# Kernel tuning notes

Hardware: AMD Instinct MI355X
Metric: run time of the kernel (lower is better)

Reference implementation:

```python
import jax, jax.numpy as jnp
import numpy as np

N, NFEAT, NHID, NHEADS, OUT_DIM = 4096, 512, 64, 8, 512
ALPHA = 0.2      # LeakyReLU negative slope
NEG = -9e15      # masked-out logit value (as in pyGAT)


def setup_inputs() -> dict:
    key = jax.random.key(0)
    ks = jax.random.split(key, 10)
    s = 0.1
    x = jax.random.normal(ks[0], (N, NFEAT), jnp.float32)
    adj = jax.random.randint(ks[1], (N, N), 0, 2, jnp.int32)  # dense 0/1 adjacency
    W1 = jax.random.normal(ks[2], (NHEADS, NFEAT, NHID), jnp.float32) * s
    a1 = jax.random.normal(ks[3], (NHEADS, 2 * NHID), jnp.float32) * s
    Wo = jax.random.normal(ks[4], (NHEADS * NHID, OUT_DIM), jnp.float32) * s
    ao = jax.random.normal(ks[5], (2 * OUT_DIM,), jnp.float32) * s
    lin1_w = jax.random.normal(ks[6], (OUT_DIM, 1024), jnp.float32) * s
    lin1_b = jnp.zeros((1024,), jnp.float32)
    lin2_w = jax.random.normal(ks[7], (1024, 512), jnp.float32) * s
    lin2_b = jnp.zeros((512,), jnp.float32)
    return dict(x=x, adj=adj, W1=W1, a1=a1, Wo=Wo, ao=ao,
                lin1_w=lin1_w, lin1_b=lin1_b, lin2_w=lin2_w, lin2_b=lin2_b)


def _gat_heads(x, adj_mask, W, a):
    # Dense pyGAT GraphAttentionLayer, vectorized over heads.
    # W: [H, F, O], a: [H, 2O], x: [N, F], adj_mask: [N, N] bool
    O = W.shape[-1]
    Wh = jnp.einsum('nf,hfo->hno', x, W)                      # [H, N, O]
    src = jnp.einsum('hno,ho->hn', Wh, a[:, :O])              # a_1^T Wh_i
    dst = jnp.einsum('hno,ho->hn', Wh, a[:, O:])              # a_2^T Wh_j
    e = jax.nn.leaky_relu(src[:, :, None] + dst[:, None, :], ALPHA)  # [H, N, N]
    e = jnp.where(adj_mask[None, :, :], e, NEG)
    attn = jax.nn.softmax(e, axis=-1)
    return jnp.einsum('hnm,hmo->hno', attn, Wh)               # [H, N, O]


def reference(x, adj, W1, a1, Wo, ao, lin1_w, lin1_b, lin2_w, lin2_b):
    mask = adj > 0
    # layer-1 heads (concat=True -> elu per head), then concat along features
    h = jax.nn.elu(_gat_heads(x, mask, W1, a1))               # [H, N, NHID]
    x1 = jnp.transpose(h, (1, 0, 2)).reshape(x.shape[0], -1)  # [N, H*NHID]
    # output attention head (concat=False -> raw h'), elu applied in GAT.forward
    h2 = _gat_heads(x1, mask, Wo[None], ao[None])[0]          # [N, OUT_DIM]
    out = jax.nn.elu(h2)
    out = jax.nn.relu(out @ lin1_w + lin1_b)                  # Linear(out_dim,1024)+ReLU
    return out @ lin2_w + lin2_b                              # Linear(1024,512)
```

## Files before the change

kernel.cpp:

```cpp
#include <hip/hip_runtime.h>

#define NN 4096
#define NFEAT 512
#define NHID 64
#define NHEADS 8
#define OUTD 512
#define LRALPHA 0.2f
#define NSPLIT 2
#define JS (NN / NSPLIT)
#define JTILES (JS / 64)

typedef __attribute__((ext_vector_type(4))) float f32x4;
typedef __attribute__((ext_vector_type(8))) short short8;
typedef __attribute__((ext_vector_type(4))) int   int4v;
typedef __attribute__((ext_vector_type(2))) unsigned uint2v;

#define OFF_BITS (size_t)0x0
#define OFF_WHA  (size_t)0x200000
#define OFF_SRC  (size_t)0xA00000
#define OFF_DST  (size_t)0xA20000
#define OFF_MDM  (size_t)0xA40000
#define OFF_MDD  (size_t)0xA80000
#define OFF_XHH  (size_t)0xAC0000
#define OFF_XHL  (size_t)0xEC0000
#define OFF_WHH  (size_t)0x12C0000
#define OFF_WHL  (size_t)0x16C0000
#define OFF_PART (size_t)0x1AC0000
#define OFF_L1OH OFF_PART
#define OFF_L1OL (OFF_PART + (size_t)0x800000)
#define OFF_W1TH (size_t)0x2AC0000
#define OFF_W1TL (size_t)0x2B40000
#define OFF_WOTH (size_t)0x2BC0000
#define OFF_WOTL (size_t)0x2C40000
#define OFF_L1WH (size_t)0x2CC0000
#define OFF_L1WL (size_t)0x2DC0000
#define OFF_L2WH (size_t)0x2EC0000
#define OFF_L2WL (size_t)0x2FC0000

__device__ inline unsigned short f2bf(float x) {
    unsigned u = __float_as_uint(x);
    return (unsigned short)((u + 0x7FFFu + ((u >> 16) & 1u)) >> 16);
}

#define PACK_PAIR(ve, vo, hw_, lw_) {                                   \
    unsigned ue = __float_as_uint(ve), uo = __float_as_uint(vo);        \
    unsigned ho = uo & 0xFFFF0000u;                                     \
    hw_ = (int)(ho | (ue >> 16));                                       \
    float le_ = (ve) - __uint_as_float(ue & 0xFFFF0000u);               \
    float lo_ = (vo) - __uint_as_float(ho);                             \
    lw_ = (int)((__float_as_uint(lo_) & 0xFFFF0000u) |                  \
                (__float_as_uint(le_) >> 16)); }

__global__ __launch_bounds__(256) void pack_bits_kernel(
    const int* __restrict__ adj, unsigned int* __restrict__ bits)
{
    int wid  = (blockIdx.x * 256 + threadIdx.x) >> 6;
    int lane = threadIdx.x & 63;
    int row  = wid >> 6;
    int j0   = (wid & 63) << 6;
    int v    = adj[(long)row * NN + j0 + lane];
    unsigned long long m = __ballot(v > 0);
    if (lane == 0)  bits[row * 128 + (j0 >> 5)]     = (unsigned int)m;
    if (lane == 32) bits[row * 128 + (j0 >> 5) + 1] = (unsigned int)(m >> 32);
}

__global__ __launch_bounds__(256) void splitA_kernel(
    const float* __restrict__ in, unsigned short* __restrict__ oh,
    unsigned short* __restrict__ ol)
{
    long i = ((long)blockIdx.x * 256 + threadIdx.x) * 8;
    float4 a = *(const float4*)&in[i], b = *(const float4*)&in[i + 4];
    float v[8] = {a.x, a.y, a.z, a.w, b.x, b.y, b.z, b.w};
    int4v hw, lw;
    #pragma unroll
    for (int pp = 0; pp < 4; ++pp) PACK_PAIR(v[2*pp], v[2*pp+1], hw[pp], lw[pp]);
    *(short8*)&oh[i] = __builtin_bit_cast(short8, hw);
    *(short8*)&ol[i] = __builtin_bit_cast(short8, lw);
}

__global__ __launch_bounds__(256) void splitBT_kernel(
    const float* __restrict__ B, unsigned short* __restrict__ oh,
    unsigned short* __restrict__ ol, int K, int N, long srcZ, long dstZ)
{
    __shared__ float tile[64][65];
    const int t = threadIdx.x;
    const int n0 = blockIdx.x * 64, k0 = blockIdx.y * 64;
    B  += srcZ * blockIdx.z;
    oh += dstZ * blockIdx.z;
    ol += dstZ * blockIdx.z;
    #pragma unroll
    for (int it = 0; it < 4; ++it) {
        int k = it * 16 + (t >> 4);
        *(float4*)&tile[k][(t & 15) * 4] =
            *(const float4*)&B[(long)(k0 + k) * N + n0 + (t & 15) * 4];
    }
    __syncthreads();
    const int n = t >> 2, kc = (t & 3) * 16;
    #pragma unroll
    for (int g = 0; g < 2; ++g) {
        int4v hw, lw;
        #pragma unroll
        for (int pp = 0; pp < 4; ++pp) {
            float ve = tile[kc + g * 8 + 2 * pp][n];
            float vo = tile[kc + g * 8 + 2 * pp + 1][n];
            PACK_PAIR(ve, vo, hw[pp], lw[pp]);
        }
        long ob = (long)(n0 + n) * K + k0 + kc + g * 8;
        *(short8*)&oh[ob] = __builtin_bit_cast(short8, hw);
        *(short8*)&ol[ob] = __builtin_bit_cast(short8, lw);
    }
}

template<int WF32, int WSPL, int DO_BIAS, int DO_RELU>
__global__ __launch_bounds__(256, 3) void mgemm_kernel(
    const unsigned short* __restrict__ Ah, const unsigned short* __restrict__ Al,
    const unsigned short* __restrict__ Bh, const unsigned short* __restrict__ Bl,
    float* __restrict__ C, unsigned short* __restrict__ Ch,
    unsigned short* __restrict__ Cl, const float* __restrict__ bias,
    int N, int K, long bZ, long cZ)
{
    __shared__ unsigned short AH[2][4096], AL[2][4096];
    __shared__ unsigned short BH[2][2048], BL[2][2048];

    const int t = threadIdx.x;
    const int m0 = blockIdx.x * 128, n0 = blockIdx.y * 64;
    Bh += bZ * blockIdx.z; Bl += bZ * blockIdx.z;
    if (WF32) C += cZ * blockIdx.z;

    const int ar0 = t >> 2, ar1 = 64 + (t >> 2), akb = t & 3;
    const unsigned short* pAh = Ah + (long)(m0 + ar0) * K + akb * 8;
    const unsigned short* pAl = Al + (long)(m0 + ar0) * K + akb * 8;
    const unsigned short* pBh = Bh + (long)(n0 + ar0) * K + akb * 8;
    const unsigned short* pBl = Bl + (long)(n0 + ar0) * K + akb * 8;
    const long aRow1 = (long)64 * K;
    const int adst0 = ar0 * 32 + ((akb ^ ((ar0 >> 1) & 3)) << 3);
    const int adst1 = ar1 * 32 + ((akb ^ ((ar1 >> 1) & 3)) << 3);
    const int bdst  = adst0;

    short8 sh0, sh1, sl0, sl1, sbh, sbl;
    const int S = K / 32;

#define MG_LOAD(s) { long o = (long)(s) * 32;                     \
        sh0 = *(const short8*)(pAh + o);                          \
        sh1 = *(const short8*)(pAh + aRow1 + o);                  \
        sl0 = *(const short8*)(pAl + o);                          \
        sl1 = *(const short8*)(pAl + aRow1 + o);                  \
        sbh = *(const short8*)(pBh + o);                          \
        sbl = *(const short8*)(pBl + o); }
#define MG_COMMIT(b) {                                            \
        *(short8*)&AH[b][adst0] = sh0; *(short8*)&AH[b][adst1] = sh1; \
        *(short8*)&AL[b][adst0] = sl0; *(short8*)&AL[b][adst1] = sl1; \
        *(short8*)&BH[b][bdst]  = sbh; *(short8*)&BL[b][bdst]  = sbl; }

    MG_LOAD(0);
    MG_COMMIT(0);
    if (S > 1) MG_LOAD(1);
    __syncthreads();

    const int w = t >> 6, l = t & 63;
    const int kb = l >> 4;
    const int r0 = w * 32 + (l & 15), r1 = r0 + 16;
    const int ao0 = r0 * 32 + ((kb ^ ((r0 >> 1) & 3)) << 3);
    const int ao1 = r1 * 32 + ((kb ^ ((r1 >> 1) & 3)) << 3);

    f32x4 acc0[4] = {}, acc1[4] = {};

    for (int s = 0; s < S; ++s) {
        const int cur = s & 1;
        if (s + 1 < S) MG_COMMIT(cur ^ 1);
        if (s + 2 < S) MG_LOAD(s + 2);

        short8 a0h = *(const short8*)&AH[cur][ao0];
        short8 a0l = *(const short8*)&AL[cur][ao0];
        short8 a1h = *(const short8*)&AH[cur][ao1];
        short8 a1l = *(const short8*)&AL[cur][ao1];
        #pragma unroll
        for (int ct = 0; ct < 4; ++ct) {
            const int n = ct * 16 + (l & 15);
            const int bo = n * 32 + ((kb ^ ((n >> 1) & 3)) << 3);
            short8 bh = *(const short8*)&BH[cur][bo];
            short8 bl = *(const short8*)&BL[cur][bo];
            acc0[ct] = __builtin_amdgcn_mfma_f32_16x16x32_bf16(a0h, bh, acc0[ct], 0, 0, 0);
            acc0[ct] = __builtin_amdgcn_mfma_f32_16x16x32_bf16(a0h, bl, acc0[ct], 0, 0, 0);
            acc0[ct] = __builtin_amdgcn_mfma_f32_16x16x32_bf16(a0l, bh, acc0[ct], 0, 0, 0);
            acc1[ct] = __builtin_amdgcn_mfma_f32_16x16x32_bf16(a1h, bh, acc1[ct], 0, 0, 0);
            acc1[ct] = __builtin_amdgcn_mfma_f32_16x16x32_bf16(a1h, bl, acc1[ct], 0, 0, 0);
            acc1[ct] = __builtin_amdgcn_mfma_f32_16x16x32_bf16(a1l, bh, acc1[ct], 0, 0, 0);
        }
        __syncthreads();
    }
#undef MG_LOAD
#undef MG_COMMIT

    #pragma unroll
    for (int rs = 0; rs < 2; ++rs) {
        #pragma unroll
        for (int ct = 0; ct < 4; ++ct) {
            const int col = n0 + ct * 16 + (l & 15);
            float b = DO_BIAS ? bias[col] : 0.f;
            f32x4 av = rs ? acc1[ct] : acc0[ct];
            #pragma unroll
            for (int g = 0; g < 4; ++g) {
                int row = m0 + w * 32 + rs * 16 + (l >> 4) * 4 + g;
                float v = av[g] + b;
                if (DO_RELU) v = v > 0.f ? v : 0.f;
                if (WF32) C[(long)row * N + col] = v;
                if (WSPL) {
                    unsigned u = __float_as_uint(v);
                    Ch[(long)row * N + col] = (unsigned short)(u >> 16);
                    float lo = v - __uint_as_float(u & 0xFFFF0000u);
                    Cl[(long)row * N + col] = (unsigned short)(__float_as_uint(lo) >> 16);
                }
            }
        }
    }
}

__global__ __launch_bounds__(256) void srcdst_kernel(
    const float* __restrict__ Wh, const float* __restrict__ a,
    float* __restrict__ src, float* __restrict__ dst, int HN, int Nn, int O)
{
    int wid  = (blockIdx.x * 256 + threadIdx.x) >> 6;
    int lane = threadIdx.x & 63;
    if (wid >= HN) return;
    int h = wid / Nn;
    const float* row = Wh + (long)wid * O;
    const float* ah  = a + (long)h * 2 * O;
    float s = 0.f, d = 0.f;
    for (int o = lane; o < O; o += 64) {
        float v = row[o];
        s += v * ah[o];
        d += v * ah[O + o];
    }
    #pragma unroll
    for (int off = 32; off > 0; off >>= 1) {
        s += __shfl_xor(s, off);
        d += __shfl_xor(d, off);
    }
    if (lane == 0) { src[wid] = s; dst[wid] = d; }
}

__global__ __launch_bounds__(256) void whsplit_kernel(
    const float* __restrict__ Wh, long yStride, int ldJ,
    unsigned short* __restrict__ outH, unsigned short* __restrict__ outL)
{
    __shared__ float tile[64][68];
    const int t = threadIdx.x;
    const int j0 = blockIdx.x * 64;
    const int y = blockIdx.y;
    #pragma unroll
    for (int p = 0; p < 4; ++p) {
        int j = p * 16 + (t >> 4);
        int c = (t & 15) * 4;
        *(float4*)&tile[j][c] =
            *(const float4*)&Wh[(long)(j0 + j) * ldJ + (long)y * yStride + c];
    }
    __syncthreads();
    const int c = t >> 2, jb = (t & 3) * 16;
    short8 H0, H1, L0, L1;
    #pragma unroll
    for (int e = 0; e < 8; ++e) {
        float v = tile[jb + e][c];
        unsigned short h = f2bf(v);
        H0[e] = (short)h;
        L0[e] = (short)f2bf(v - __uint_as_float((unsigned)h << 16));
    }
    #pragma unroll
    for (int e = 0; e < 8; ++e) {
        float v = tile[jb + 8 + e][c];
        unsigned short h = f2bf(v);
        H1[e] = (short)h;
        L1[e] = (short)f2bf(v - __uint_as_float((unsigned)h << 16));
    }
    long ob = (long)y * 262144 + (long)c * 4096 + j0 + jb;
    *(short8*)&outH[ob]     = H0;
    *(short8*)&outH[ob + 8] = H1;
    *(short8*)&outL[ob]     = L0;
    *(short8*)&outL[ob + 8] = L1;
}

__global__ __launch_bounds__(512, 4) void attn_kernel(
    const unsigned short* __restrict__ whH, const unsigned short* __restrict__ whL,
    const float* __restrict__ src, const float* __restrict__ dst, int snOff_y,
    const unsigned int* __restrict__ bits,
    float* __restrict__ partA, float* __restrict__ md_m, float* __restrict__ md_d)
{
    __shared__ unsigned short BH[2][4096];
    __shared__ unsigned short BL[2][4096];
    __shared__ float dstS[JS];
    __shared__ float srcS[128], mS[128];

    const int t  = threadIdx.x;
    const int i0 = blockIdx.x * 128;
    const int y  = blockIdx.y;
    const int js = blockIdx.z;
    src += (long)snOff_y * y;
    dst += (long)snOff_y * y;

    const int sc = t >> 3, sb = t & 7;
    const long gbase = (long)y * 262144 + (long)sc * 4096 + js * JS + sb * 8;
    const int sdst = sc * 64 + ((sb ^ (sc & 7)) << 3);

    short8 stH = *(const short8*)(whH + gbase);
    short8 stL = *(const short8*)(whL + gbase);

    *(float4*)&dstS[t * 4] = *(const float4*)&dst[js * JS + t * 4];
    if (t < 128) srcS[t] = src[i0 + t];
    __syncthreads();

    {
        const int r = t >> 2, q = t & 3;
        float md = -3.0e38f;
        const unsigned int* brow = bits + (long)(i0 + r) * 128 + js * (JS / 32) + q * 16;
        for (int wi = 0; wi < 16; ++wi) {
            unsigned int b = brow[wi];
            if (!b) continue;
            int base = q * 512 + wi * 32;
            while (b) {
                int bi = __ffs(b) - 1; b &= b - 1;
                float v = dstS[base + bi];
                md = v > md ? v : md;
            }
        }
        md = fmaxf(md, __shfl_xor(md, 1));
        md = fmaxf(md, __shfl_xor(md, 2));
        if (q == 0) {
            float m;
            if (md < -2.9e38f) m = -2.0e38f;
            else { float e = srcS[r] + md; m = e > 0.f ? e : LRALPHA * e; }
            mS[r] = m;
        }
    }
    *(short8*)&BH[0][sdst] = stH;
    *(short8*)&BL[0][sdst] = stL;
    stH = *(const short8*)(whH + gbase + 64);
    stL = *(const short8*)(whL + gbase + 64);
    __syncthreads();

    const int w = t >> 6, l = t & 63;
    const int rA = 16 * w + (l & 15);
    const int q8 = (l >> 4) * 8;
    const float src_r = srcS[rA];
    const float m_r   = mS[rA];
    const bool  empty = (m_r <= -1.9e38f);
    const unsigned int* browp = bits + (long)(i0 + rA) * 128 + js * (JS / 32);
    const short8 ONES = {(short)0x3F80, (short)0x3F80, (short)0x3F80, (short)0x3F80,
                         (short)0x3F80, (short)0x3F80, (short)0x3F80, (short)0x3F80};

    f32x4 acc[4] = {};
    f32x4 acc_d = {};

    for (int jt = 0; jt < JTILES; ++jt) {
        const int cur = jt & 1;
        if (jt + 1 < JTILES) {
            *(short8*)&BH[cur ^ 1][sdst] = stH;
            *(short8*)&BL[cur ^ 1][sdst] = stL;
        }
        if (jt + 2 < JTILES) {
            stH = *(const short8*)(whH + gbase + (jt + 2) * 64);
            stL = *(const short8*)(whL + gbase + (jt + 2) * 64);
        }
        unsigned int bw0 = browp[jt * 2], bw1 = browp[jt * 2 + 1];
        short8 aH0, aL0, aH1, aL1;
        #pragma unroll
        for (int kt = 0; kt < 2; ++kt) {
            unsigned int bw = kt ? bw1 : bw0;
            float4 d0 = *(const float4*)&dstS[jt * 64 + kt * 32 + q8];
            float4 d1 = *(const float4*)&dstS[jt * 64 + kt * 32 + q8 + 4];
            float dv[8] = {d0.x, d0.y, d0.z, d0.w, d1.x, d1.y, d1.z, d1.w};
            float pv[8];
            #pragma unroll
            for (int e = 0; e < 8; ++e) {
                float v = src_r + dv[e];
                v = fmaxf(v, LRALPHA * v);
                float pe = __expf(v - m_r);
                bool valid = (bw >> (q8 + e)) & 1u;
                pv[e] = empty ? 1.f : (valid ? pe : 0.f);
            }
            int4v hw, lw;
            #pragma unroll
            for (int pp = 0; pp < 4; ++pp) PACK_PAIR(pv[2*pp], pv[2*pp+1], hw[pp], lw[pp]);
            short8 aH = __builtin_bit_cast(short8, hw);
            short8 aL = __builtin_bit_cast(short8, lw);
            acc_d = __builtin_amdgcn_mfma_f32_16x16x32_bf16(aH, ONES, acc_d, 0, 0, 0);
            acc_d = __builtin_amdgcn_mfma_f32_16x16x32_bf16(aL, ONES, acc_d, 0, 0, 0);
            if (kt == 0) { aH0 = aH; aL0 = aL; } else { aH1 = aH; aL1 = aL; }
        }
        #pragma unroll
        for (int kt = 0; kt < 2; ++kt) {
            short8 aH = kt ? aH1 : aH0;
            short8 aL = kt ? aL1 : aL0;
            #pragma unroll
            for (int ct = 0; ct < 4; ++ct) {
                const int c = ct * 16 + (l & 15);
                const int off = c * 64 + ((((kt * 4) + (l >> 4)) ^ (c & 7)) << 3);
                short8 bh = *(const short8*)&BH[cur][off];
                short8 bl = *(const short8*)&BL[cur][off];
                acc[ct] = __builtin_amdgcn_mfma_f32_16x16x32_bf16(aH, bh, acc[ct], 0, 0, 0);
                acc[ct] = __builtin_amdgcn_mfma_f32_16x16x32_bf16(aH, bl, acc[ct], 0, 0, 0);
                acc[ct] = __builtin_amdgcn_mfma_f32_16x16x32_bf16(aL, bh, acc[ct], 0, 0, 0);
            }
        }
        __syncthreads();
    }

    const int colb = y * 64 + (l & 15);
    #pragma unroll
    for (int ct = 0; ct < 4; ++ct) {
        #pragma unroll
        for (int g = 0; g < 4; ++g) {
            int row = 16 * w + (l >> 4) * 4 + g;
            partA[((long)js * NN + i0 + row) * OUTD + colb + ct * 16] = acc[ct][g];
        }
    }
    if ((l & 15) == 0) {
        long mdoff = ((long)js * NHEADS + y) * NN + i0 + 16 * w + (l >> 4) * 4;
        #pragma unroll
        for (int g = 0; g < 4; ++g) md_d[mdoff + g] = acc_d[g];
    }
    if (l < 16) {
        md_m[((long)js * NHEADS + y) * NN + i0 + 16 * w + l] = m_r;
    }
}

__global__ __launch_bounds__(256) void combine_kernel(
    const float* __restrict__ partA, const float* __restrict__ md_m,
    const float* __restrict__ md_d, unsigned short* __restrict__ outH,
    unsigned short* __restrict__ outL)
{
    int idx4 = (blockIdx.x * 256 + threadIdx.x) * 4;
    int row  = idx4 >> 9;
    int col  = idx4 & 511;
    int slot = col >> 6;
    float m[NSPLIT], w[NSPLIT];
    float M = -3.4e38f;
    #pragma unroll
    for (int s = 0; s < NSPLIT; ++s) {
        m[s] = md_m[((long)s * NHEADS + slot) * NN + row];
        M = fmaxf(M, m[s]);
    }
    float den = 0.f;
    #pragma unroll
    for (int s = 0; s < NSPLIT; ++s) {
        w[s] = __expf(m[s] - M);
        den += w[s] * md_d[((long)s * NHEADS + slot) * NN + row];
    }
    float4 num = {0.f, 0.f, 0.f, 0.f};
    #pragma unroll
    for (int s = 0; s < NSPLIT; ++s) {
        float4 a = *(const float4*)&partA[((long)s * NN + row) * OUTD + col];
        num.x += w[s] * a.x; num.y += w[s] * a.y;
        num.z += w[s] * a.z; num.w += w[s] * a.w;
    }
    float inv = 1.f / den;
    float o[4]; const float* pn = &num.x;
    #pragma unroll
    for (int j = 0; j < 4; ++j) {
        float v = pn[j] * inv;
        o[j] = v > 0.f ? v : (__expf(v) - 1.f);
    }
    int h0, h1, l0, l1;
    PACK_PAIR(o[0], o[1], h0, l0);
    PACK_PAIR(o[2], o[3], h1, l1);
    uint2v hv = {(unsigned)h0, (unsigned)h1};
    uint2v lv = {(unsigned)l0, (unsigned)l1};
    *(uint2v*)&outH[(long)row * OUTD + col] = hv;
    *(uint2v*)&outL[(long)row * OUTD + col] = lv;
}

extern "C" void kernel_launch(void* const* d_in, const int* in_sizes, int n_in,
                              void* d_out, int out_size, void* d_ws, size_t ws_size,
                              hipStream_t stream) {
    const float* x   = (const float*)d_in[0];
    const int*   adj = (const int*)d_in[1];
    const float* W1  = (const float*)d_in[2];
    const float* a1  = (const float*)d_in[3];
    const float* Wo  = (const float*)d_in[4];
    const float* ao  = (const float*)d_in[5];
    const float* l1w = (const float*)d_in[6];
    const float* l1b = (const float*)d_in[7];
    const float* l2w = (const float*)d_in[8];
    const float* l2b = (const float*)d_in[9];
    float* out = (float*)d_out;

    char* ws = (char*)d_ws;
    unsigned int* bits = (unsigned int*)(ws + OFF_BITS);
    float* WhA  = (float*)(ws + OFF_WHA);
    float* srcB = (float*)(ws + OFF_SRC);
    float* dstB = (float*)(ws + OFF_DST);
    float* mdm  = (float*)(ws + OFF_MDM);
    float* mdd  = (float*)(ws + OFF_MDD);
    unsigned short* xhH = (unsigned short*)(ws + OFF_XHH);
    unsigned short* xhL = (unsigned short*)(ws + OFF_XHL);
    unsigned short* whH = (unsigned short*)(ws + OFF_WHH);
    unsigned short* whL = (unsigned short*)(ws + OFF_WHL);
    float* part = (float*)(ws + OFF_PART);
    unsigned short* l1oH = (unsigned short*)(ws + OFF_L1OH);
    unsigned short* l1oL = (unsigned short*)(ws + OFF_L1OL);
    unsigned short* w1tH = (unsigned short*)(ws + OFF_W1TH);
    unsigned short* w1tL = (unsigned short*)(ws + OFF_W1TL);
    unsigned short* wotH = (unsigned short*)(ws + OFF_WOTH);
    unsigned short* wotL = (unsigned short*)(ws + OFF_WOTL);
    unsigned short* l1wH = (unsigned short*)(ws + OFF_L1WH);
    unsigned short* l1wL = (unsigned short*)(ws + OFF_L1WL);
    unsigned short* l2wH = (unsigned short*)(ws + OFF_L2WH);
    unsigned short* l2wL = (unsigned short*)(ws + OFF_L2WL);

    pack_bits_kernel<<<65536, 256, 0, stream>>>(adj, bits);
    splitA_kernel<<<1024, 256, 0, stream>>>(x, xhH, xhL);
    splitBT_kernel<<<dim3(1, 8, 8), 256, 0, stream>>>(W1, w1tH, w1tL, NFEAT, NHID,
        (long)NFEAT * NHID, (long)NHID * NFEAT);
    splitBT_kernel<<<dim3(8, 8, 1), 256, 0, stream>>>(Wo, wotH, wotL, 512, OUTD, 0, 0);
    splitBT_kernel<<<dim3(16, 8, 1), 256, 0, stream>>>(l1w, l1wH, l1wL, OUTD, 1024, 0, 0);
    splitBT_kernel<<<dim3(8, 16, 1), 256, 0, stream>>>(l2w, l2wH, l2wL, 1024, OUTD, 0, 0);

    mgemm_kernel<1,0,0,0><<<dim3(32, 1, 8), 256, 0, stream>>>(
        xhH, xhL, w1tH, w1tL, WhA, nullptr, nullptr, nullptr,
        NHID, NFEAT, (long)NHID * NFEAT, (long)NN * NHID);
    srcdst_kernel<<<8192, 256, 0, stream>>>(WhA, a1, srcB, dstB, NHEADS*NN, NN, NHID);
    whsplit_kernel<<<dim3(64, 8), 256, 0, stream>>>(WhA, (long)NN*NHID, NHID, whH, whL);
    attn_kernel<<<dim3(32, 8, NSPLIT), 512, 0, stream>>>(
        whH, whL, srcB, dstB, NN, bits, part, mdm, mdd);
    combine_kernel<<<2048, 256, 0, stream>>>(part, mdm, mdd, xhH, xhL);
    mgemm_kernel<1,0,0,0><<<dim3(32, 8, 1), 256, 0, stream>>>(
        xhH, xhL, wotH, wotL, WhA, nullptr, nullptr, nullptr, OUTD, 512, 0, 0);
    srcdst_kernel<<<1024, 256, 0, stream>>>(WhA, ao, srcB, dstB, NN, NN, OUTD);
    whsplit_kernel<<<dim3(64, 8), 256, 0, stream>>>(WhA, 64L, OUTD, whH, whL);
    attn_kernel<<<dim3(32, 8, NSPLIT), 512, 0, stream>>>(
        whH, whL, srcB, dstB, 0, bits, part, mdm, mdd);
    combine_kernel<<<2048, 256, 0, stream>>>(part, mdm, mdd, xhH, xhL);
    mgemm_kernel<0,1,1,1><<<dim3(32, 16, 1), 256, 0, stream>>>(
        xhH, xhL, l1wH, l1wL, nullptr, l1oH, l1oL, l1b, 1024, OUTD, 0, 0);
    mgemm_kernel<1,0,1,0><<<dim3(32, 8, 1), 256, 0, stream>>>(
        l1oH, l1oL, l2wH, l2wL, out, nullptr, nullptr, l2b, OUTD, 1024, 0, 0);
}
```

Before: 462.5 us.

## Fuse src/dst and bf16 split into GEMM epilogue, widen attention split, use exp2

The Wh GEMM epilogue now computes the attention src/dst dot products (pre-scaled by log2e) and writes the transposed bf16 hi/lo split directly, removing the separate srcdst and whsplit kernels and the fp32 Wh round trip. The output layer accumulates src/dst with atomics into a buffer zeroed by a new kernel. The attention j-range is split four ways when the workspace is large enough, which raises parallelism at the cost of more combine traffic. Float-to-bf16 packing switches to the hardware packed-convert instruction, and the exponentials use exp2 with masking folded into the exponent argument.

```diff
diff --git a/kernel.cpp b/kernel.cpp
--- a/kernel.cpp
+++ b/kernel.cpp
@@ -6,9 +6,7 @@
 #define NHEADS 8
 #define OUTD 512
 #define LRALPHA 0.2f
-#define NSPLIT 2
-#define JS (NN / NSPLIT)
-#define JTILES (JS / 64)
+#define LOG2E 1.4426950408889634f
 
 typedef __attribute__((ext_vector_type(4))) float f32x4;
 typedef __attribute__((ext_vector_type(8))) short short8;
@@ -16,40 +14,48 @@
 typedef __attribute__((ext_vector_type(2))) unsigned uint2v;
 
 #define OFF_BITS (size_t)0x0
-#define OFF_WHA  (size_t)0x200000
-#define OFF_SRC  (size_t)0xA00000
-#define OFF_DST  (size_t)0xA20000
-#define OFF_MDM  (size_t)0xA40000
-#define OFF_MDD  (size_t)0xA80000
-#define OFF_XHH  (size_t)0xAC0000
-#define OFF_XHL  (size_t)0xEC0000
-#define OFF_WHH  (size_t)0x12C0000
-#define OFF_WHL  (size_t)0x16C0000
-#define OFF_PART (size_t)0x1AC0000
+#define OFF_XHH  (size_t)0x200000
+#define OFF_XHL  (size_t)0x600000
+#define OFF_WHH  (size_t)0xA00000
+#define OFF_WHL  (size_t)0xE00000
+#define OFF_W1TH (size_t)0x1200000
+#define OFF_W1TL (size_t)0x1280000
+#define OFF_WOTH (size_t)0x1300000
+#define OFF_WOTL (size_t)0x1380000
+#define OFF_L1WH (size_t)0x1400000
+#define OFF_L1WL (size_t)0x1500000
+#define OFF_L2WH (size_t)0x1600000
+#define OFF_L2WL (size_t)0x1700000
+#define OFF_SRC  (size_t)0x1800000
+#define OFF_DST  (size_t)0x1820000
+#define OFF_SRC2 (size_t)0x1840000
+#define OFF_DST2 (size_t)0x1844000
+#define OFF_MDM  (size_t)0x1850000
+#define OFF_MDD  (size_t)0x18D0000
+#define OFF_PART (size_t)0x1950000
 #define OFF_L1OH OFF_PART
 #define OFF_L1OL (OFF_PART + (size_t)0x800000)
-#define OFF_W1TH (size_t)0x2AC0000
-#define OFF_W1TL (size_t)0x2B40000
-#define OFF_WOTH (size_t)0x2BC0000
-#define OFF_WOTL (size_t)0x2C40000
-#define OFF_L1WH (size_t)0x2CC0000
-#define OFF_L1WL (size_t)0x2DC0000
-#define OFF_L2WH (size_t)0x2EC0000
-#define OFF_L2WL (size_t)0x2FC0000
-
-__device__ inline unsigned short f2bf(float x) {
-    unsigned u = __float_as_uint(x);
-    return (unsigned short)((u + 0x7FFFu + ((u >> 16) & 1u)) >> 16);
-}
-
-#define PACK_PAIR(ve, vo, hw_, lw_) {                                   \
-    unsigned ue = __float_as_uint(ve), uo = __float_as_uint(vo);        \
-    unsigned ho = uo & 0xFFFF0000u;                                     \
-    hw_ = (int)(ho | (ue >> 16));                                       \
-    float le_ = (ve) - __uint_as_float(ue & 0xFFFF0000u);               \
-    float lo_ = (vo) - __uint_as_float(ho);                             \
-    lw_ = (int)((__float_as_uint(lo_) & 0xFFFF0000u) |                  \
-                (__float_as_uint(le_) >> 16)); }
+#define WS_NEED4 (OFF_PART + (size_t)0x2000000)
+#define WS_NEED2 (OFF_PART + (size_t)0x1000000)
+
+__device__ inline unsigned cvt_pk_bf16(float lo, float hi) {
+    unsigned r;
+    asm("v_cvt_pk_bf16_f32 %0, %1, %2" : "=v"(r) : "v"(lo), "v"(hi));
+    return r;
+}
+__device__ inline void pack_pair(float ve, float vo, unsigned& hw, unsigned& lw) {
+    hw = cvt_pk_bf16(ve, vo);
+    float he = __uint_as_float(hw << 16);
+    float ho = __uint_as_float(hw & 0xFFFF0000u);
+    lw = cvt_pk_bf16(ve - he, vo - ho);
+}
+__device__ inline float exp2_fast(float x) {
+#if __has_builtin(__builtin_amdgcn_exp2f)
+    return __builtin_amdgcn_exp2f(x);
+#else
+    float r; asm("v_exp_f32 %0, %1" : "=v"(r) : "v"(x)); return r;
+#endif
+}
 
 __global__ __launch_bounds__(256) void pack_bits_kernel(
     const int* __restrict__ adj, unsigned int* __restrict__ bits)
@@ -64,6 +70,13 @@
     if (lane == 32) bits[row * 128 + (j0 >> 5) + 1] = (unsigned int)(m >> 32);
 }
 
+__global__ __launch_bounds__(256) void zero_kernel(float* __restrict__ a,
+                                                   float* __restrict__ b)
+{
+    int i = blockIdx.x * 256 + threadIdx.x;
+    if (i < NN) { a[i] = 0.f; b[i] = 0.f; }
+}
+
 __global__ __launch_bounds__(256) void splitA_kernel(
     const float* __restrict__ in, unsigned short* __restrict__ oh,
     unsigned short* __restrict__ ol)
@@ -73,7 +86,10 @@
     float v[8] = {a.x, a.y, a.z, a.w, b.x, b.y, b.z, b.w};
     int4v hw, lw;
     #pragma unroll
-    for (int pp = 0; pp < 4; ++pp) PACK_PAIR(v[2*pp], v[2*pp+1], hw[pp], lw[pp]);
+    for (int pp = 0; pp < 4; ++pp) {
+        unsigned h, l; pack_pair(v[2*pp], v[2*pp+1], h, l);
+        hw[pp] = (int)h; lw[pp] = (int)l;
+    }
     *(short8*)&oh[i] = __builtin_bit_cast(short8, hw);
     *(short8*)&ol[i] = __builtin_bit_cast(short8, lw);
 }
@@ -101,9 +117,9 @@
         int4v hw, lw;
         #pragma unroll
         for (int pp = 0; pp < 4; ++pp) {
-            float ve = tile[kc + g * 8 + 2 * pp][n];
-            float vo = tile[kc + g * 8 + 2 * pp + 1][n];
-            PACK_PAIR(ve, vo, hw[pp], lw[pp]);
+            unsigned h, l;
+            pack_pair(tile[kc + g*8 + 2*pp][n], tile[kc + g*8 + 2*pp + 1][n], h, l);
+            hw[pp] = (int)h; lw[pp] = (int)l;
         }
         long ob = (long)(n0 + n) * K + k0 + kc + g * 8;
         *(short8*)&oh[ob] = __builtin_bit_cast(short8, hw);
@@ -111,21 +127,23 @@
     }
 }
 
-template<int WF32, int WSPL, int DO_BIAS, int DO_RELU>
+template<int EPI, int DO_BIAS, int DO_RELU>
 __global__ __launch_bounds__(256, 3) void mgemm_kernel(
     const unsigned short* __restrict__ Ah, const unsigned short* __restrict__ Al,
     const unsigned short* __restrict__ Bh, const unsigned short* __restrict__ Bl,
     float* __restrict__ C, unsigned short* __restrict__ Ch,
     unsigned short* __restrict__ Cl, const float* __restrict__ bias,
-    int N, int K, long bZ, long cZ)
+    const float* __restrict__ avec, float* __restrict__ srcO, float* __restrict__ dstO,
+    unsigned short* __restrict__ tH, unsigned short* __restrict__ tL,
+    int N, int K, long bZ, long cZ, int aoff)
 {
     __shared__ unsigned short AH[2][4096], AL[2][4096];
-    __shared__ unsigned short BH[2][2048], BL[2][2048];
+    __shared__ unsigned short BHs[2][2048], BLs[2][2048];
 
     const int t = threadIdx.x;
     const int m0 = blockIdx.x * 128, n0 = blockIdx.y * 64;
-    Bh += bZ * blockIdx.z; Bl += bZ * blockIdx.z;
-    if (WF32) C += cZ * blockIdx.z;
+    const int zi = blockIdx.z;
+    Bh += bZ * zi; Bl += bZ * zi;
 
     const int ar0 = t >> 2, ar1 = 64 + (t >> 2), akb = t & 3;
     const unsigned short* pAh = Ah + (long)(m0 + ar0) * K + akb * 8;
@@ -135,7 +153,6 @@
     const long aRow1 = (long)64 * K;
     const int adst0 = ar0 * 32 + ((akb ^ ((ar0 >> 1) & 3)) << 3);
     const int adst1 = ar1 * 32 + ((akb ^ ((ar1 >> 1) & 3)) << 3);
-    const int bdst  = adst0;
 
     short8 sh0, sh1, sl0, sl1, sbh, sbl;
     const int S = K / 32;
@@ -150,7 +167,7 @@
 #define MG_COMMIT(b) {                                            \
         *(short8*)&AH[b][adst0] = sh0; *(short8*)&AH[b][adst1] = sh1; \
         *(short8*)&AL[b][adst0] = sl0; *(short8*)&AL[b][adst1] = sl1; \
-        *(short8*)&BH[b][bdst]  = sbh; *(short8*)&BL[b][bdst]  = sbl; }
+        *(short8*)&BHs[b][adst0] = sbh; *(short8*)&BLs[b][adst0] = sbl; }
 
     MG_LOAD(0);
     MG_COMMIT(0);
@@ -178,8 +195,8 @@
         for (int ct = 0; ct < 4; ++ct) {
             const int n = ct * 16 + (l & 15);
             const int bo = n * 32 + ((kb ^ ((n >> 1) & 3)) << 3);
-            short8 bh = *(const short8*)&BH[cur][bo];
-            short8 bl = *(const short8*)&BL[cur][bo];
+            short8 bh = *(const short8*)&BHs[cur][bo];
+            short8 bl = *(const short8*)&BLs[cur][bo];
             acc0[ct] = __builtin_amdgcn_mfma_f32_16x16x32_bf16(a0h, bh, acc0[ct], 0, 0, 0);
             acc0[ct] = __builtin_amdgcn_mfma_f32_16x16x32_bf16(a0h, bl, acc0[ct], 0, 0, 0);
             acc0[ct] = __builtin_amdgcn_mfma_f32_16x16x32_bf16(a0l, bh, acc0[ct], 0, 0, 0);
@@ -192,102 +209,98 @@
 #undef MG_LOAD
 #undef MG_COMMIT
 
-    #pragma unroll
-    for (int rs = 0; rs < 2; ++rs) {
+    if constexpr (EPI <= 1) {
+        #pragma unroll
+        for (int rs = 0; rs < 2; ++rs) {
+            #pragma unroll
+            for (int ct = 0; ct < 4; ++ct) {
+                const int col = n0 + ct * 16 + (l & 15);
+                float b = DO_BIAS ? bias[col] : 0.f;
+                f32x4 av = rs ? acc1[ct] : acc0[ct];
+                #pragma unroll
+                for (int g = 0; g < 4; ++g) {
+                    int row = m0 + w * 32 + rs * 16 + (l >> 4) * 4 + g;
+                    float v = av[g] + b;
+                    if (DO_RELU) v = v > 0.f ? v : 0.f;
+                    if (EPI == 0) C[cZ * zi + (long)row * N + col] = v;
+                    else {
+                        unsigned u = __float_as_uint(v);
+                        Ch[(long)row * N + col] = (unsigned short)((u + 0x7FFFu + ((u >> 16) & 1u)) >> 16);
+                        unsigned hh = (u + 0x7FFFu + ((u >> 16) & 1u)) & 0xFFFF0000u;
+                        float hf = __uint_as_float(((u + 0x7FFFu + ((u >> 16) & 1u)) >> 16) << 16);
+                        float lo = v - hf;
+                        unsigned ul = __float_as_uint(lo);
+                        Cl[(long)row * N + col] = (unsigned short)((ul + 0x7FFFu + ((ul >> 16) & 1u)) >> 16);
+                        (void)hh;
+                    }
+                }
+            }
+        }
+    } else {
+        float avs[4], avd[4];
         #pragma unroll
         for (int ct = 0; ct < 4; ++ct) {
-            const int col = n0 + ct * 16 + (l & 15);
-            float b = DO_BIAS ? bias[col] : 0.f;
-            f32x4 av = rs ? acc1[ct] : acc0[ct];
+            int col = n0 + ct * 16 + (l & 15);
+            avs[ct] = avec[(EPI == 2 ? zi * 2 * 64 : 0) + col];
+            avd[ct] = avec[(EPI == 2 ? zi * 2 * 64 : 0) + aoff + col];
+        }
+        #pragma unroll
+        for (int rs = 0; rs < 2; ++rs) {
+            const int rbase = m0 + w * 32 + rs * 16 + (l >> 4) * 4;
+            #pragma unroll
+            for (int ct = 0; ct < 4; ++ct) {
+                const int col = n0 + ct * 16 + (l & 15);
+                f32x4 av = rs ? acc1[ct] : acc0[ct];
+                unsigned h0, l0, h1, l1;
+                pack_pair(av[0], av[1], h0, l0);
+                pack_pair(av[2], av[3], h1, l1);
+                long tb = (EPI == 2 ? (long)zi * 262144 + (long)col * 4096
+                                    : (long)(col >> 6) * 262144 + (long)(col & 63) * 4096)
+                          + rbase;
+                uint2v hv = {h0, h1}, lv = {l0, l1};
+                *(uint2v*)&tH[tb] = hv;
+                *(uint2v*)&tL[tb] = lv;
+            }
             #pragma unroll
             for (int g = 0; g < 4; ++g) {
-                int row = m0 + w * 32 + rs * 16 + (l >> 4) * 4 + g;
-                float v = av[g] + b;
-                if (DO_RELU) v = v > 0.f ? v : 0.f;
-                if (WF32) C[(long)row * N + col] = v;
-                if (WSPL) {
-                    unsigned u = __float_as_uint(v);
-                    Ch[(long)row * N + col] = (unsigned short)(u >> 16);
-                    float lo = v - __uint_as_float(u & 0xFFFF0000u);
-                    Cl[(long)row * N + col] = (unsigned short)(__float_as_uint(lo) >> 16);
+                float sd = 0.f, dd = 0.f;
+                #pragma unroll
+                for (int ct = 0; ct < 4; ++ct) {
+                    f32x4 av = rs ? acc1[ct] : acc0[ct];
+                    sd += av[g] * avs[ct];
+                    dd += av[g] * avd[ct];
                 }
-            }
-        }
-    }
-}
-
-__global__ __launch_bounds__(256) void srcdst_kernel(
-    const float* __restrict__ Wh, const float* __restrict__ a,
-    float* __restrict__ src, float* __restrict__ dst, int HN, int Nn, int O)
-{
-    int wid  = (blockIdx.x * 256 + threadIdx.x) >> 6;
-    int lane = threadIdx.x & 63;
-    if (wid >= HN) return;
-    int h = wid / Nn;
-    const float* row = Wh + (long)wid * O;
-    const float* ah  = a + (long)h * 2 * O;
-    float s = 0.f, d = 0.f;
-    for (int o = lane; o < O; o += 64) {
-        float v = row[o];
-        s += v * ah[o];
-        d += v * ah[O + o];
-    }
-    #pragma unroll
-    for (int off = 32; off > 0; off >>= 1) {
-        s += __shfl_xor(s, off);
-        d += __shfl_xor(d, off);
-    }
-    if (lane == 0) { src[wid] = s; dst[wid] = d; }
-}
-
-__global__ __launch_bounds__(256) void whsplit_kernel(
-    const float* __restrict__ Wh, long yStride, int ldJ,
-    unsigned short* __restrict__ outH, unsigned short* __restrict__ outL)
-{
-    __shared__ float tile[64][68];
-    const int t = threadIdx.x;
-    const int j0 = blockIdx.x * 64;
-    const int y = blockIdx.y;
-    #pragma unroll
-    for (int p = 0; p < 4; ++p) {
-        int j = p * 16 + (t >> 4);
-        int c = (t & 15) * 4;
-        *(float4*)&tile[j][c] =
-            *(const float4*)&Wh[(long)(j0 + j) * ldJ + (long)y * yStride + c];
-    }
-    __syncthreads();
-    const int c = t >> 2, jb = (t & 3) * 16;
-    short8 H0, H1, L0, L1;
-    #pragma unroll
-    for (int e = 0; e < 8; ++e) {
-        float v = tile[jb + e][c];
-        unsigned short h = f2bf(v);
-        H0[e] = (short)h;
-        L0[e] = (short)f2bf(v - __uint_as_float((unsigned)h << 16));
-    }
-    #pragma unroll
-    for (int e = 0; e < 8; ++e) {
-        float v = tile[jb + 8 + e][c];
-        unsigned short h = f2bf(v);
-        H1[e] = (short)h;
-        L1[e] = (short)f2bf(v - __uint_as_float((unsigned)h << 16));
-    }
-    long ob = (long)y * 262144 + (long)c * 4096 + j0 + jb;
-    *(short8*)&outH[ob]     = H0;
-    *(short8*)&outH[ob + 8] = H1;
-    *(short8*)&outL[ob]     = L0;
-    *(short8*)&outL[ob + 8] = L1;
-}
-
+                #pragma unroll
+                for (int off = 1; off < 16; off <<= 1) {
+                    sd += __shfl_xor(sd, off);
+                    dd += __shfl_xor(dd, off);
+                }
+                if ((l & 15) == 0) {
+                    int row = rbase + g;
+                    if (EPI == 2) {
+                        srcO[zi * NN + row] = sd * LOG2E;
+                        dstO[zi * NN + row] = dd * LOG2E;
+                    } else {
+                        atomicAdd(&srcO[row], sd * LOG2E);
+                        atomicAdd(&dstO[row], dd * LOG2E);
+                    }
+                }
+            }
+        }
+    }
+}
+
+template<int JS_>
 __global__ __launch_bounds__(512, 4) void attn_kernel(
     const unsigned short* __restrict__ whH, const unsigned short* __restrict__ whL,
     const float* __restrict__ src, const float* __restrict__ dst, int snOff_y,
     const unsigned int* __restrict__ bits,
     float* __restrict__ partA, float* __restrict__ md_m, float* __restrict__ md_d)
 {
+    constexpr int JT_ = JS_ / 64;
     __shared__ unsigned short BH[2][4096];
     __shared__ unsigned short BL[2][4096];
-    __shared__ float dstS[JS];
+    __shared__ float dstS[JS_];
     __shared__ float srcS[128], mS[128];
 
     const int t  = threadIdx.x;
@@ -298,24 +311,26 @@
     dst += (long)snOff_y * y;
 
     const int sc = t >> 3, sb = t & 7;
-    const long gbase = (long)y * 262144 + (long)sc * 4096 + js * JS + sb * 8;
+    const long gbase = (long)y * 262144 + (long)sc * 4096 + (long)js * JS_ + sb * 8;
     const int sdst = sc * 64 + ((sb ^ (sc & 7)) << 3);
 
     short8 stH = *(const short8*)(whH + gbase);
     short8 stL = *(const short8*)(whL + gbase);
 
-    *(float4*)&dstS[t * 4] = *(const float4*)&dst[js * JS + t * 4];
+    if (t * 4 < JS_)
+        *(float4*)&dstS[t * 4] = *(const float4*)&dst[(long)js * JS_ + t * 4];
     if (t < 128) srcS[t] = src[i0 + t];
     __syncthreads();
 
     {
+        constexpr int WPQ = JS_ / 128;
         const int r = t >> 2, q = t & 3;
         float md = -3.0e38f;
-        const unsigned int* brow = bits + (long)(i0 + r) * 128 + js * (JS / 32) + q * 16;
-        for (int wi = 0; wi < 16; ++wi) {
+        const unsigned int* brow = bits + (long)(i0 + r) * 128 + js * (JS_ / 32) + q * WPQ;
+        for (int wi = 0; wi < WPQ; ++wi) {
             unsigned int b = brow[wi];
             if (!b) continue;
-            int base = q * 512 + wi * 32;
+            int base = q * (JS_ / 4) + wi * 32;
             while (b) {
                 int bi = __ffs(b) - 1; b &= b - 1;
                 float v = dstS[base + bi];
@@ -327,7 +342,7 @@
         if (q == 0) {
             float m;
             if (md < -2.9e38f) m = -2.0e38f;
-            else { float e = srcS[r] + md; m = e > 0.f ? e : LRALPHA * e; }
+            else { float e = srcS[r] + md; m = fmaxf(e, LRALPHA * e); }
             mS[r] = m;
         }
     }
@@ -343,20 +358,20 @@
     const float src_r = srcS[rA];
     const float m_r   = mS[rA];
     const bool  empty = (m_r <= -1.9e38f);
-    const unsigned int* browp = bits + (long)(i0 + rA) * 128 + js * (JS / 32);
+    const unsigned int* browp = bits + (long)(i0 + rA) * 128 + js * (JS_ / 32);
     const short8 ONES = {(short)0x3F80, (short)0x3F80, (short)0x3F80, (short)0x3F80,
                          (short)0x3F80, (short)0x3F80, (short)0x3F80, (short)0x3F80};
 
     f32x4 acc[4] = {};
     f32x4 acc_d = {};
 
-    for (int jt = 0; jt < JTILES; ++jt) {
+    for (int jt = 0; jt < JT_; ++jt) {
         const int cur = jt & 1;
-        if (jt + 1 < JTILES) {
+        if (jt + 1 < JT_) {
             *(short8*)&BH[cur ^ 1][sdst] = stH;
             *(short8*)&BL[cur ^ 1][sdst] = stL;
         }
-        if (jt + 2 < JTILES) {
+        if (jt + 2 < JT_) {
             stH = *(const short8*)(whH + gbase + (jt + 2) * 64);
             stL = *(const short8*)(whL + gbase + (jt + 2) * 64);
         }
@@ -373,13 +388,18 @@
             for (int e = 0; e < 8; ++e) {
                 float v = src_r + dv[e];
                 v = fmaxf(v, LRALPHA * v);
-                float pe = __expf(v - m_r);
+                float s = v - m_r;
                 bool valid = (bw >> (q8 + e)) & 1u;
-                pv[e] = empty ? 1.f : (valid ? pe : 0.f);
+                s = valid ? s : -1.0e30f;
+                s = empty ? 0.f : s;
+                pv[e] = exp2_fast(s);
             }
             int4v hw, lw;
             #pragma unroll
-            for (int pp = 0; pp < 4; ++pp) PACK_PAIR(pv[2*pp], pv[2*pp+1], hw[pp], lw[pp]);
+            for (int pp = 0; pp < 4; ++pp) {
+                unsigned h, lo; pack_pair(pv[2*pp], pv[2*pp+1], h, lo);
+                hw[pp] = (int)h; lw[pp] = (int)lo;
+            }
             short8 aH = __builtin_bit_cast(short8, hw);
             short8 aL = __builtin_bit_cast(short8, lw);
             acc_d = __builtin_amdgcn_mfma_f32_16x16x32_bf16(aH, ONES, acc_d, 0, 0, 0);
@@ -423,6 +443,7 @@
     }
 }
 
+template<int NS>
 __global__ __launch_bounds__(256) void combine_kernel(
     const float* __restrict__ partA, const float* __restrict__ md_m,
     const float* __restrict__ md_d, unsigned short* __restrict__ outH,
@@ -432,22 +453,22 @@
     int row  = idx4 >> 9;
     int col  = idx4 & 511;
     int slot = col >> 6;
-    float m[NSPLIT], w[NSPLIT];
+    float m[NS], w[NS];
     float M = -3.4e38f;
     #pragma unroll
-    for (int s = 0; s < NSPLIT; ++s) {
+    for (int s = 0; s < NS; ++s) {
         m[s] = md_m[((long)s * NHEADS + slot) * NN + row];
         M = fmaxf(M, m[s]);
     }
     float den = 0.f;
     #pragma unroll
-    for (int s = 0; s < NSPLIT; ++s) {
-        w[s] = __expf(m[s] - M);
+    for (int s = 0; s < NS; ++s) {
+        w[s] = exp2_fast(m[s] - M);
         den += w[s] * md_d[((long)s * NHEADS + slot) * NN + row];
     }
     float4 num = {0.f, 0.f, 0.f, 0.f};
     #pragma unroll
-    for (int s = 0; s < NSPLIT; ++s) {
+    for (int s = 0; s < NS; ++s) {
         float4 a = *(const float4*)&partA[((long)s * NN + row) * OUTD + col];
         num.x += w[s] * a.x; num.y += w[s] * a.y;
         num.z += w[s] * a.z; num.w += w[s] * a.w;
@@ -459,11 +480,10 @@
         float v = pn[j] * inv;
         o[j] = v > 0.f ? v : (__expf(v) - 1.f);
     }
-    int h0, h1, l0, l1;
-    PACK_PAIR(o[0], o[1], h0, l0);
-    PACK_PAIR(o[2], o[3], h1, l1);
-    uint2v hv = {(unsigned)h0, (unsigned)h1};
-    uint2v lv = {(unsigned)l0, (unsigned)l1};
+    unsigned h0, l0, h1, l1;
+    pack_pair(o[0], o[1], h0, l0);
+    pack_pair(o[2], o[3], h1, l1);
+    uint2v hv = {h0, h1}, lv = {l0, l1};
     *(uint2v*)&outH[(long)row * OUTD + col] = hv;
     *(uint2v*)&outL[(long)row * OUTD + col] = lv;
 }
@@ -485,18 +505,10 @@
 
     char* ws = (char*)d_ws;
     unsigned int* bits = (unsigned int*)(ws + OFF_BITS);
-    float* WhA  = (float*)(ws + OFF_WHA);
-    float* srcB = (float*)(ws + OFF_SRC);
-    float* dstB = (float*)(ws + OFF_DST);
-    float* mdm  = (float*)(ws + OFF_MDM);
-    float* mdd  = (float*)(ws + OFF_MDD);
     unsigned short* xhH = (unsigned short*)(ws + OFF_XHH);
     unsigned short* xhL = (unsigned short*)(ws + OFF_XHL);
     unsigned short* whH = (unsigned short*)(ws + OFF_WHH);
     unsigned short* whL = (unsigned short*)(ws + OFF_WHL);
-    float* part = (float*)(ws + OFF_PART);
-    unsigned short* l1oH = (unsigned short*)(ws + OFF_L1OH);
-    unsigned short* l1oL = (unsigned short*)(ws + OFF_L1OL);
     unsigned short* w1tH = (unsigned short*)(ws + OFF_W1TH);
     unsigned short* w1tL = (unsigned short*)(ws + OFF_W1TL);
     unsigned short* wotH = (unsigned short*)(ws + OFF_WOTH);
@@ -505,8 +517,20 @@
     unsigned short* l1wL = (unsigned short*)(ws + OFF_L1WL);
     unsigned short* l2wH = (unsigned short*)(ws + OFF_L2WH);
     unsigned short* l2wL = (unsigned short*)(ws + OFF_L2WL);
+    float* srcB = (float*)(ws + OFF_SRC);
+    float* dstB = (float*)(ws + OFF_DST);
+    float* src2 = (float*)(ws + OFF_SRC2);
+    float* dst2 = (float*)(ws + OFF_DST2);
+    float* mdm  = (float*)(ws + OFF_MDM);
+    float* mdd  = (float*)(ws + OFF_MDD);
+    float* part = (float*)(ws + OFF_PART);
+    unsigned short* l1oH = (unsigned short*)(ws + OFF_L1OH);
+    unsigned short* l1oL = (unsigned short*)(ws + OFF_L1OL);
+
+    const int nsplit = (ws_size >= WS_NEED4) ? 4 : 2;
 
     pack_bits_kernel<<<65536, 256, 0, stream>>>(adj, bits);
+    zero_kernel<<<16, 256, 0, stream>>>(src2, dst2);
     splitA_kernel<<<1024, 256, 0, stream>>>(x, xhH, xhL);
     splitBT_kernel<<<dim3(1, 8, 8), 256, 0, stream>>>(W1, w1tH, w1tL, NFEAT, NHID,
         (long)NFEAT * NHID, (long)NHID * NFEAT);
@@ -514,23 +538,34 @@
     splitBT_kernel<<<dim3(16, 8, 1), 256, 0, stream>>>(l1w, l1wH, l1wL, OUTD, 1024, 0, 0);
     splitBT_kernel<<<dim3(8, 16, 1), 256, 0, stream>>>(l2w, l2wH, l2wL, 1024, OUTD, 0, 0);
 
-    mgemm_kernel<1,0,0,0><<<dim3(32, 1, 8), 256, 0, stream>>>(
-        xhH, xhL, w1tH, w1tL, WhA, nullptr, nullptr, nullptr,
-        NHID, NFEAT, (long)NHID * NFEAT, (long)NN * NHID);
-    srcdst_kernel<<<8192, 256, 0, stream>>>(WhA, a1, srcB, dstB, NHEADS*NN, NN, NHID);
-    whsplit_kernel<<<dim3(64, 8), 256, 0, stream>>>(WhA, (long)NN*NHID, NHID, whH, whL);
-    attn_kernel<<<dim3(32, 8, NSPLIT), 512, 0, stream>>>(
-        whH, whL, srcB, dstB, NN, bits, part, mdm, mdd);
-    combine_kernel<<<2048, 256, 0, stream>>>(part, mdm, mdd, xhH, xhL);
-    mgemm_kernel<1,0,0,0><<<dim3(32, 8, 1), 256, 0, stream>>>(
-        xhH, xhL, wotH, wotL, WhA, nullptr, nullptr, nullptr, OUTD, 512, 0, 0);
-    srcdst_kernel<<<1024, 256, 0, stream>>>(WhA, ao, srcB, dstB, NN, NN, OUTD);
-    whsplit_kernel<<<dim3(64, 8), 256, 0, stream>>>(WhA, 64L, OUTD, whH, whL);
-    attn_kernel<<<dim3(32, 8, NSPLIT), 512, 0, stream>>>(
-        whH, whL, srcB, dstB, 0, bits, part, mdm, mdd);
-    combine_kernel<<<2048, 256, 0, stream>>>(part, mdm, mdd, xhH, xhL);
-    mgemm_kernel<0,1,1,1><<<dim3(32, 16, 1), 256, 0, stream>>>(
-        xhH, xhL, l1wH, l1wL, nullptr, l1oH, l1oL, l1b, 1024, OUTD, 0, 0);
-    mgemm_kernel<1,0,1,0><<<dim3(32, 8, 1), 256, 0, stream>>>(
-        l1oH, l1oL, l2wH, l2wL, out, nullptr, nullptr, l2b, OUTD, 1024, 0, 0);
-}
+    mgemm_kernel<2,0,0><<<dim3(32, 1, 8), 256, 0, stream>>>(
+        xhH, xhL, w1tH, w1tL, nullptr, nullptr, nullptr, nullptr,
+        a1, srcB, dstB, whH, whL, NHID, NFEAT, (long)NHID * NFEAT, 0, 64);
+    if (nsplit == 4) {
+        attn_kernel<1024><<<dim3(32, 8, 4), 512, 0, stream>>>(
+            whH, whL, srcB, dstB, NN, bits, part, mdm, mdd);
+        combine_kernel<4><<<2048, 256, 0, stream>>>(part, mdm, mdd, xhH, xhL);
+    } else {
+        attn_kernel<2048><<<dim3(32, 8, 2), 512, 0, stream>>>(
+            whH, whL, srcB, dstB, NN, bits, part, mdm, mdd);
+        combine_kernel<2><<<2048, 256, 0, stream>>>(part, mdm, mdd, xhH, xhL);
+    }
+    mgemm_kernel<3,0,0><<<dim3(32, 8, 1), 256, 0, stream>>>(
+        xhH, xhL, wotH, wotL, nullptr, nullptr, nullptr, nullptr,
+        ao, src2, dst2, whH, whL, OUTD, 512, 0, 0, 512);
+    if (nsplit == 4) {
+        attn_kernel<1024><<<dim3(32, 8, 4), 512, 0, stream>>>(
+            whH, whL, src2, dst2, 0, bits, part, mdm, mdd);
+        combine_kernel<4><<<2048, 256, 0, stream>>>(part, mdm, mdd, xhH, xhL);
+    } else {
+        attn_kernel<2048><<<dim3(32, 8, 2), 512, 0, stream>>>(
+            whH, whL, src2, dst2, 0, bits, part, mdm, mdd);
+        combine_kernel<2><<<2048, 256, 0, stream>>>(part, mdm, mdd, xhH, xhL);
+    }
+    mgemm_kernel<1,1,1><<<dim3(32, 16, 1), 256, 0, stream>>>(
+        xhH, xhL, l1wH, l1wL, nullptr, l1oH, l1oL, l1b,
+        nullptr, nullptr, nullptr, nullptr, nullptr, 1024, OUTD, 0, 0, 0);
+    mgemm_kernel<0,1,0><<<dim3(32, 8, 1), 256, 0, stream>>>(
+        l1oH, l1oL, l2wH, l2wL, out, nullptr, nullptr, l2b,
+        nullptr, nullptr, nullptr, nullptr, nullptr, OUTD, 1024, 0, 0, 0);
+}
```

Result: faster. 431.6 us (-6.7%).
